# Optimization experiments

Measured on AMD Instinct MI355X. Metric: run time of the kernel, lower is better.

Reference implementation:

```python
import jax, jax.numpy as jnp
import numpy as np

K = 3                 # patch / kernel size (ksize)
SOFTMAX_SCALE = 10.0
RES_SCALE = 1.0
EPS = 1e-4            # escape_NaN


def prelu(x, a):
    # nn.PReLU() with a single learnable parameter a (shape [1])
    return jnp.where(x >= 0, x, a * x)


def conv1x1_prelu(x, w, b, a):
    # x: [N,C,H,W], w: [O,C], b: [O] -- 1x1 conv + PReLU (BasicBlock)
    y = jnp.einsum('nchw,oc->nohw', x, w) + b[None, :, None, None]
    return prelu(y, a)


def extract_patches(x):
    # SAME-padded 3x3 patch extraction, stride 1 (torch Unfold ordering: C,kh,kw)
    # x: [N,C,H,W] -> [N, H*W, C*9]
    N, C, H, W = x.shape
    xp = jnp.pad(x, ((0, 0), (0, 0), (1, 1), (1, 1)))
    p = jnp.stack([jnp.stack([xp[:, :, i:i + H, j:j + W] for j in range(K)], axis=2)
                   for i in range(K)], axis=2)          # [N,C,3,3,H,W] (i outer -> kh)
    return p.reshape(N, C * K * K, H * W).transpose(0, 2, 1)


def pyramid_attention(input_l, input_s, w_mlb, b_mlb, a_mlb, w_m, b_m, a_m, w_asm, b_asm, a_asm):
    N, _, H_l, W_l = input_l.shape
    _, _, H_s, W_s = input_s.shape
    L = H_s * W_s

    match_base = conv1x1_prelu(input_l, w_mlb, b_mlb, a_mlb)   # [N,32,H_l,W_l]
    base = conv1x1_prelu(input_s, w_asm, b_asm, a_asm)          # [N,64,H_s,W_s]
    ref = conv1x1_prelu(input_s, w_m, b_m, a_m)                 # [N,32,H_s,W_s]

    # key patches from ref, L2-normalized per patch (wi / (||wi|| + eps))
    w_patch = extract_patches(ref)                              # [N, L, 32*9]
    norm = jnp.sqrt(jnp.sum(w_patch * w_patch, axis=-1, keepdims=True)) + EPS
    w_normed = w_patch / norm

    # query patches from match_base (same padding), correlation == patch matmul
    x_patch = extract_patches(match_base)                       # [N, H_l*W_l, 32*9]
    scores = jnp.einsum('bpk,blk->bpl', x_patch, w_normed) * SOFTMAX_SCALE
    attn = jax.nn.softmax(scores, axis=-1)                      # softmax over L keys
    attn = attn.transpose(0, 2, 1).reshape(N, L, H_l, W_l)

    # value patches from base; conv_transpose2d(stride=1, padding=1) == conv with
    # spatially-flipped kernel and in/out channels swapped, SAME padding
    raw_w = extract_patches(base).reshape(N, L, 64, K, K)       # [N,L,64,3,3]
    w_ct = jnp.flip(raw_w, axis=(-2, -1)).transpose(0, 2, 1, 3, 4)  # [N,64,L,3,3]

    def per_sample(a, k):
        return jax.lax.conv_general_dilated(
            a[None], k, window_strides=(1, 1), padding=[(1, 1), (1, 1)],
            dimension_numbers=('NCHW', 'OIHW', 'NCHW'))[0]

    y = jax.vmap(per_sample)(attn, w_ct) / 4.0                  # [N,64,H_l,W_l]
    return y + input_l * RES_SCALE


def setup_inputs() -> dict:
    key = jax.random.key(0)
    ks = jax.random.split(key, 12)
    N, C, H_l, W_l, H_s, W_s = 4, 64, 96, 96, 48, 48
    Cr = C // 2  # reduction=2
    return {
        'input_l': jax.random.normal(ks[0], (N, C, H_l, W_l), jnp.float32),
        'input_s': jax.random.normal(ks[1], (N, C, H_s, W_s), jnp.float32),
        'w_mlb': jax.random.normal(ks[2], (Cr, C), jnp.float32) * 0.05,
        'b_mlb': jax.random.normal(ks[3], (Cr,), jnp.float32) * 0.01,
        'a_mlb': jnp.full((1,), 0.25, jnp.float32),
        'w_m': jax.random.normal(ks[4], (Cr, C), jnp.float32) * 0.05,
        'b_m': jax.random.normal(ks[5], (Cr,), jnp.float32) * 0.01,
        'a_m': jnp.full((1,), 0.25, jnp.float32),
        'w_asm': jax.random.normal(ks[6], (C, C), jnp.float32) * 0.05,
        'b_asm': jax.random.normal(ks[7], (C,), jnp.float32) * 0.01,
        'a_asm': jnp.full((1,), 0.25, jnp.float32),
    }


def reference(input_l, input_s, w_mlb, b_mlb, a_mlb, w_m, b_m, a_m, w_asm, b_asm, a_asm):
    return pyramid_attention(input_l, input_s, w_mlb, b_mlb, a_mlb,
                             w_m, b_m, a_m, w_asm, b_asm, a_asm)
```

## Files before the change

### kernel.cpp

```cpp
#include <hip/hip_runtime.h>
#include <hip/hip_bf16.h>
#include <cstdint>
#include <cstddef>

typedef __hip_bfloat16 bf16;
using short8 = __attribute__((ext_vector_type(8))) short;
using f32x4  = __attribute__((ext_vector_type(4))) float;
using float4v = __attribute__((ext_vector_type(4))) float;
using uint4v  = __attribute__((ext_vector_type(4))) unsigned int;

__device__ __forceinline__ float s2f(short s) {
  unsigned u = ((unsigned)(unsigned short)s) << 16;
  return __builtin_bit_cast(float, u);
}
__device__ __forceinline__ short f2s(float f) {
  unsigned u = __builtin_bit_cast(unsigned, f);
  u += 0x7fffu + ((u >> 16) & 1u);
  return (short)(u >> 16);
}
__device__ __forceinline__ float bclo(unsigned u) { return __builtin_bit_cast(float, u << 16); }
__device__ __forceinline__ float bchi(unsigned u) { return __builtin_bit_cast(float, u & 0xFFFF0000u); }

__global__ __launch_bounds__(256) void k_conv_all(
    const float* __restrict__ in_l, const float* __restrict__ in_s,
    const float* __restrict__ w_mlb, const float* __restrict__ b_mlb, const float* __restrict__ a_mlb,
    const float* __restrict__ w_m,   const float* __restrict__ b_m,   const float* __restrict__ a_m,
    const float* __restrict__ w_asm, const float* __restrict__ b_asm, const float* __restrict__ a_asm,
    float* __restrict__ MBpad, float* __restrict__ REFpad, float* __restrict__ BASEpad,
    int t1, int t2, int t3)
{
  int idx = blockIdx.x * 256 + threadIdx.x;
  const float *in, *w, *bi, *ap; float* o; int Cout, Hin, Win;
  if (idx < t1) { in = in_l; w = w_mlb; bi = b_mlb; ap = a_mlb; o = MBpad; Cout = 32; Hin = 96; Win = 96; }
  else if (idx < t1 + t2) { idx -= t1; in = in_s; w = w_m; bi = b_m; ap = a_m; o = REFpad; Cout = 32; Hin = 48; Win = 48; }
  else if (idx < t1 + t2 + t3) { idx -= t1 + t2; in = in_s; w = w_asm; bi = b_asm; ap = a_asm; o = BASEpad; Cout = 64; Hin = 48; Win = 48; }
  else return;
  int Wp = Win + 2, Hp = Hin + 2;
  int x = idx % Wp;
  int t = idx / Wp;
  int y = t % Hp; t /= Hp;
  int oc = t % Cout; int n = t / Cout;
  if (x == 0 || x == Wp - 1 || y == 0 || y == Hp - 1) { o[idx] = 0.0f; return; }
  int cs = Hin * Win;
  const float* ip = in + (size_t)n * 64 * cs + (size_t)(y - 1) * Win + (x - 1);
  const float* wp = w + oc * 64;
  float s = bi[oc];
#pragma unroll 16
  for (int ci = 0; ci < 64; ci++)
    s += wp[ci] * ip[(size_t)ci * cs];
  float a = ap[0];
  o[idx] = s >= 0.0f ? s : a * s;
}

__global__ __launch_bounds__(256) void k_gather_all(
    const float* __restrict__ mbpad, const float* __restrict__ refpad,
    const float* __restrict__ basepad,
    bf16* __restrict__ Kp, bf16* __restrict__ Xp, bf16* __restrict__ Bb)
{
  int b = blockIdx.x;
  int tid = threadIdx.x;
  if (b < 2304) {
    int wid = b * 4 + (tid >> 6);
    int lane = tid & 63;
    int n = wid / 2304, l = wid % 2304, lh = l / 48, lw = l % 48;
    float v[5]; float ss = 0.f;
#pragma unroll
    for (int i = 0; i < 5; i++) {
      int k = lane + 64 * i; v[i] = 0.f;
      if (k < 288) {
        int c = k / 9, rr = (k % 9) / 3, sc = k % 3;
        v[i] = refpad[((size_t)(n * 32 + c) * 50 + lh + rr) * 50 + lw + sc];
        ss += v[i] * v[i];
      }
    }
#pragma unroll
    for (int off = 32; off; off >>= 1) ss += __shfl_xor(ss, off);
    float inv = 10.f / (sqrtf(ss) + 1e-4f);
#pragma unroll
    for (int i = 0; i < 5; i++) {
      int k = lane + 64 * i;
      Kp[(size_t)wid * 320 + k] = __float2bfloat16(k < 288 ? v[i] * inv : 0.f);
    }
  } else if (b < 2304 + 46080) {
    int idx = (b - 2304) * 256 + tid;
    int k = idx % 320; int p = (idx / 320) % 9216; int n = idx / (320 * 9216);
    float val = 0.f;
    if (k < 288) {
      int c = k / 9, rr = (k % 9) / 3, sc = k % 3;
      int ph = p / 96, pw = p % 96;
      val = mbpad[((size_t)(n * 32 + c) * 98 + ph + rr) * 98 + pw + sc];
    }
    Xp[idx] = __float2bfloat16(val);
  } else {
    int idx = (b - 48384) * 256 + tid;
    int l = idx % 2304; int o = (idx / 2304) % 64; int n = idx / (2304 * 64);
    int lh = l / 48, lw = l % 48;
    Bb[idx] = __float2bfloat16(basepad[((size_t)(n * 64 + o) * 50 + lh + 1) * 50 + lw + 1]);
  }
}

__global__ __launch_bounds__(256, 3) void k_qk(
    const bf16* __restrict__ Xp, const bf16* __restrict__ Kp,
    bf16* __restrict__ attnT, float* __restrict__ statsM, float* __restrict__ statsZ,
    int nbase, int qlo)
{
  __shared__ __align__(16) short KsPs[256 * 72];
  __shared__ float Sm[2][2][32];
  __shared__ float Sz[2][2][32];
  int z = blockIdx.z;
  int n = nbase + z;
  attnT += (size_t)z * 9216 * 2304;
  statsM += (size_t)z * 9 * 9216;
  statsZ += (size_t)z * 9 * 9216;
  int tid = threadIdx.x, lane = tid & 63, wv = tid >> 6;
  int quad = lane >> 4, m16 = lane & 15;
  int wr = wv >> 1, wc = wv & 1;
  int q0 = qlo + blockIdx.x * 64;
  int l0 = blockIdx.y * 256;

  f32x4 acc[2][8];
#pragma unroll
  for (int mi = 0; mi < 2; mi++)
#pragma unroll
    for (int t = 0; t < 8; t++) acc[mi][t] = (f32x4){0.f, 0.f, 0.f, 0.f};

  const short* Xrow = (const short*)Xp + ((size_t)n * 9216 + q0 + wr * 32 + m16) * 320;
  const short* Ksrc = (const short*)Kp + ((size_t)n * 2304 + l0) * 320;
  int srow = tid >> 2;
  int scol = (tid & 3) * 16;

  short8 pf[8];
#pragma unroll
  for (int p = 0; p < 4; p++)
#pragma unroll
    for (int v = 0; v < 2; v++)
      pf[p * 2 + v] = *(const short8*)&Ksrc[(size_t)(srow + 64 * p) * 320 + scol + v * 8];

#pragma unroll
  for (int s = 0; s < 5; s++) {
    if (s) __syncthreads();
#pragma unroll
    for (int p = 0; p < 4; p++)
#pragma unroll
      for (int v = 0; v < 2; v++)
        *(short8*)&KsPs[(srow + 64 * p) * 72 + scol + v * 8] = pf[p * 2 + v];
    __syncthreads();
    short8 xa0 = *(const short8*)&Xrow[s * 64 + quad * 8];
    short8 xa1 = *(const short8*)&Xrow[16 * 320 + s * 64 + quad * 8];
    short8 xa2 = *(const short8*)&Xrow[s * 64 + 32 + quad * 8];
    short8 xa3 = *(const short8*)&Xrow[16 * 320 + s * 64 + 32 + quad * 8];
    if (s < 4) {
      int kn = (s + 1) * 64;
#pragma unroll
      for (int p = 0; p < 4; p++)
#pragma unroll
        for (int v = 0; v < 2; v++)
          pf[p * 2 + v] = *(const short8*)&Ksrc[(size_t)(srow + 64 * p) * 320 + kn + scol + v * 8];
    }
#pragma unroll
    for (int half = 0; half < 2; half++) {
      int kc = s * 64 + half * 32;
      if (kc >= 288) break;
      short8 a0 = half ? xa2 : xa0;
      short8 a1 = half ? xa3 : xa1;
#pragma unroll
      for (int t = 0; t < 8; t++) {
        short8 bfr = *(const short8*)&KsPs[(wc * 128 + t * 16 + m16) * 72 + half * 32 + quad * 8];
        acc[0][t] = __builtin_amdgcn_mfma_f32_16x16x32_bf16(a0, bfr, acc[0][t], 0, 0, 0);
        acc[1][t] = __builtin_amdgcn_mfma_f32_16x16x32_bf16(a1, bfr, acc[1][t], 0, 0, 0);
      }
    }
  }

  float mloc[2][4], zloc[2][4], scale[2][4];
#pragma unroll
  for (int mi = 0; mi < 2; mi++)
#pragma unroll
    for (int r = 0; r < 4; r++) mloc[mi][r] = -3.0e38f;
#pragma unroll
  for (int mi = 0; mi < 2; mi++)
#pragma unroll
    for (int t = 0; t < 8; t++)
#pragma unroll
      for (int r = 0; r < 4; r++) mloc[mi][r] = fmaxf(mloc[mi][r], acc[mi][t][r]);
#pragma unroll
  for (int off = 1; off < 16; off <<= 1)
#pragma unroll
    for (int mi = 0; mi < 2; mi++)
#pragma unroll
      for (int r = 0; r < 4; r++) mloc[mi][r] = fmaxf(mloc[mi][r], __shfl_xor(mloc[mi][r], off));
#pragma unroll
  for (int mi = 0; mi < 2; mi++)
#pragma unroll
    for (int r = 0; r < 4; r++) zloc[mi][r] = 0.f;
#pragma unroll
  for (int mi = 0; mi < 2; mi++)
#pragma unroll
    for (int t = 0; t < 8; t++)
#pragma unroll
      for (int r = 0; r < 4; r++) {
        float e = __expf(acc[mi][t][r] - mloc[mi][r]);
        acc[mi][t][r] = e;
        zloc[mi][r] += e;
      }
#pragma unroll
  for (int off = 1; off < 16; off <<= 1)
#pragma unroll
    for (int mi = 0; mi < 2; mi++)
#pragma unroll
      for (int r = 0; r < 4; r++) zloc[mi][r] += __shfl_xor(zloc[mi][r], off);
  if (m16 == 0) {
#pragma unroll
    for (int mi = 0; mi < 2; mi++)
#pragma unroll
      for (int r = 0; r < 4; r++) {
        int qi = mi * 16 + quad * 4 + r;
        Sm[wc][wr][qi] = mloc[mi][r];
        Sz[wc][wr][qi] = zloc[mi][r];
      }
  }
  __syncthreads();
#pragma unroll
  for (int mi = 0; mi < 2; mi++)
#pragma unroll
    for (int r = 0; r < 4; r++) {
      int qi = mi * 16 + quad * 4 + r;
      float mo = Sm[wc ^ 1][wr][qi];
      float zo = Sz[wc ^ 1][wr][qi];
      float mc = fmaxf(mloc[mi][r], mo);
      float sc = __expf(mloc[mi][r] - mc);
      scale[mi][r] = sc;
      if (m16 == 0 && wc == 0) {
        float zc = zloc[mi][r] * sc + zo * __expf(mo - mc);
        int qq = q0 + wr * 32 + qi;
        statsM[blockIdx.y * 9216 + qq] = mc;
        statsZ[blockIdx.y * 9216 + qq] = zc;
      }
    }
#pragma unroll
  for (int mi = 0; mi < 2; mi++)
#pragma unroll
    for (int t = 0; t < 8; t++)
#pragma unroll
      for (int r = 0; r < 4; r++)
        KsPs[(wr * 32 + mi * 16 + quad * 4 + r) * 264 + wc * 128 + t * 16 + m16] =
            f2s(acc[mi][t][r] * scale[mi][r]);
  __syncthreads();
  {
    int row = tid >> 2, part = tid & 3;
    short* dst = (short*)attnT + (size_t)(q0 - qlo + row) * 2304 + l0 + part * 64;
    const short* sp = &KsPs[row * 264 + part * 64];
#pragma unroll
    for (int v = 0; v < 8; v++)
      *(short8*)&dst[v * 8] = *(const short8*)&sp[v * 8];
  }
}

__global__ __launch_bounds__(256) void k_alpha(
    const float* __restrict__ statsM, const float* __restrict__ statsZ,
    float* __restrict__ alpha, int qlo, int qlen)
{
  int z = blockIdx.y;
  statsM += (size_t)z * 9 * 9216;
  statsZ += (size_t)z * 9 * 9216;
  alpha  += (size_t)z * 9 * 9216;
  int i = blockIdx.x * 256 + threadIdx.x;
  if (i >= qlen) return;
  int q = qlo + i;
  float M = -3.0e38f;
#pragma unroll
  for (int c = 0; c < 9; c++) M = fmaxf(M, statsM[c * 9216 + q]);
  float Z = 0.f;
#pragma unroll
  for (int c = 0; c < 9; c++) Z += statsZ[c * 9216 + q] * __expf(statsM[c * 9216 + q] - M);
  float invZ = 1.f / Z;
#pragma unroll
  for (int c = 0; c < 9; c++) alpha[c * 9216 + q] = __expf(statsM[c * 9216 + q] - M) * invZ;
}

__global__ __launch_bounds__(256) void k_a2(
    const bf16* __restrict__ attnT, const float* __restrict__ alpha,
    bf16* __restrict__ A2, int q0, int qlo)
{
  int z = blockIdx.z;
  attnT += (size_t)z * 9216 * 2304;
  alpha += (size_t)z * 9 * 9216;
  A2    += (size_t)z * 9216 * 2304;
  int bpx = gridDim.x >> 3;
  int nb = (blockIdx.x & 7) * bpx + (blockIdx.x >> 3);
  int g = nb * 256 + threadIdx.x;
  int qrel = g / 144;
  int j = g - qrel * 144;
  int l0 = j * 16;
  int q = q0 + qrel;
  int h = q / 96, w = q - h * 96;
  int lh = l0 / 48, lw0 = l0 - lh * 48;
  const short* att = (const short*)attnT;
  float acc[16];
#pragma unroll
  for (int k = 0; k < 16; k++) acc[k] = 0.f;
#pragma unroll
  for (int di = -1; di <= 1; di++) {
    int hh = h + di, lhh = lh + di;
    if (hh < 0 || hh >= 96 || lhh < 0 || lhh >= 48) continue;
    int lb = l0 + 48 * di;
    int qv = q + 96 * di;
    const short* r0 = att + (size_t)(qv - qlo) * 2304;
    int c0 = lb >> 8;
    const float* alc = alpha + c0 * 9216;
    {
      float a = alc[qv];
      uint4v Va = *(const uint4v*)(r0 + lb);
      uint4v Vb = *(const uint4v*)(r0 + lb + 8);
#pragma unroll
      for (int k = 0; k < 4; k++) {
        acc[2 * k]      += bclo(Va[k]) * a;  acc[2 * k + 1]  += bchi(Va[k]) * a;
        acc[8 + 2 * k]  += bclo(Vb[k]) * a;  acc[9 + 2 * k]  += bchi(Vb[k]) * a;
      }
    }
    if (w > 0) {
      const short* rm = r0 - 2304;
      int qp = qv - 1;
      float am = alc[qp];
      float a0 = ((lb & 255) == 0 && c0 > 0) ? alpha[(c0 - 1) * 9216 + qp] : am;
      uint4v Ma = *(const uint4v*)(rm + lb);
      uint4v Mb = *(const uint4v*)(rm + lb + 8);
      unsigned P = *(const unsigned*)(rm + lb - 2);
      unsigned D[8] = { Ma[0], Ma[1], Ma[2], Ma[3], Mb[0], Mb[1], Mb[2], Mb[3] };
      unsigned E0 = (P >> 16) | (D[0] << 16);
      if (lw0 == 0) E0 &= 0xFFFF0000u;
      acc[0] += bclo(E0) * a0;  acc[1] += bchi(E0) * am;
#pragma unroll
      for (int k = 1; k < 8; k++) {
        unsigned Ek = (D[k - 1] >> 16) | (D[k] << 16);
        acc[2 * k] += bclo(Ek) * am;  acc[2 * k + 1] += bchi(Ek) * am;
      }
    }
    if (w < 95) {
      const short* rp = r0 + 2304;
      int qp = qv + 1;
      float am = alc[qp];
      float a15 = ((lb & 255) == 240 && c0 < 8) ? alpha[(c0 + 1) * 9216 + qp] : am;
      uint4v Pa = *(const uint4v*)(rp + lb);
      uint4v Pb = *(const uint4v*)(rp + lb + 8);
      unsigned N = *(const unsigned*)(rp + lb + 16);
      unsigned D[9] = { Pa[0], Pa[1], Pa[2], Pa[3], Pb[0], Pb[1], Pb[2], Pb[3], N };
      unsigned F7 = (D[7] >> 16) | (D[8] << 16);
      if (lw0 == 32) F7 &= 0x0000FFFFu;
#pragma unroll
      for (int k = 0; k < 7; k++) {
        unsigned Fk = (D[k] >> 16) | (D[k + 1] << 16);
        acc[2 * k] += bclo(Fk) * am;  acc[2 * k + 1] += bchi(Fk) * am;
      }
      acc[14] += bclo(F7) * am;  acc[15] += bchi(F7) * a15;
    }
  }
  short8 o0, o1;
#pragma unroll
  for (int k = 0; k < 8; k++) { o0[k] = f2s(acc[k]); o1[k] = f2s(acc[8 + k]); }
  short* dst = (short*)A2 + (size_t)qrel * 2304 + l0;
  *(short8*)dst = o0;
  *(short8*)(dst + 8) = o1;
}

__global__ __launch_bounds__(256) void k_pv3(
    const bf16* __restrict__ A2, const bf16* __restrict__ Bb,
    const float* __restrict__ inl, float* __restrict__ out,
    int nbase, int q0base)
{
  __shared__ float Cred[4][16][67];
  int z = blockIdx.z;
  int n = nbase + z;
  A2 += (size_t)z * 9216 * 2304;
  int tid = threadIdx.x, lane = tid & 63, wv = tid >> 6;
  int quad = lane >> 4, m16 = lane & 15;
  int qb = blockIdx.x * 16;
  int kbase = wv * 576;
  f32x4 acc[4];
#pragma unroll
  for (int t = 0; t < 4; t++) acc[t] = (f32x4){0.f, 0.f, 0.f, 0.f};

  const short* Ap = (const short*)A2 + (size_t)qb * 2304 + kbase;
  const short* Bp = (const short*)Bb + (size_t)n * 64 * 2304 + kbase;

#pragma unroll
  for (int it = 0; it < 9; it++) {
    int kw = it * 64;
#pragma unroll
    for (int ks = 0; ks < 64; ks += 32) {
      short8 a = *(const short8*)&Ap[(size_t)m16 * 2304 + kw + ks + quad * 8];
#pragma unroll
      for (int ni = 0; ni < 4; ni++) {
        short8 b = *(const short8*)&Bp[(size_t)(ni * 16 + m16) * 2304 + kw + ks + quad * 8];
        acc[ni] = __builtin_amdgcn_mfma_f32_16x16x32_bf16(a, b, acc[ni], 0, 0, 0);
      }
    }
  }
#pragma unroll
  for (int ni = 0; ni < 4; ni++)
#pragma unroll
    for (int r = 0; r < 4; r++)
      Cred[wv][quad * 4 + r][ni * 16 + m16] = acc[ni][r];
  __syncthreads();
  {
    int o = tid >> 2;
    int qg = (tid & 3) * 4;
    float4v s;
#pragma unroll
    for (int j = 0; j < 4; j++)
      s[j] = Cred[0][qg + j][o] + Cred[1][qg + j][o] + Cred[2][qg + j][o] + Cred[3][qg + j][o];
    size_t oid = ((size_t)(n * 64 + o)) * 9216 + q0base + qb + qg;
    float4v r4 = *(const float4v*)&inl[oid];
    float4v y;
#pragma unroll
    for (int j = 0; j < 4; j++) y[j] = 0.25f * s[j] + r4[j];
    *(float4v*)&out[oid] = y;
  }
}

extern "C" void kernel_launch(void* const* d_in, const int* in_sizes, int n_in,
                              void* d_out, int out_size, void* d_ws, size_t ws_size,
                              hipStream_t stream)
{
  (void)in_sizes; (void)n_in; (void)out_size;
  const float* input_l = (const float*)d_in[0];
  const float* input_s = (const float*)d_in[1];
  const float* w_mlb = (const float*)d_in[2];
  const float* b_mlb = (const float*)d_in[3];
  const float* a_mlb = (const float*)d_in[4];
  const float* w_m   = (const float*)d_in[5];
  const float* b_m   = (const float*)d_in[6];
  const float* a_m   = (const float*)d_in[7];
  const float* w_asm = (const float*)d_in[8];
  const float* b_asm = (const float*)d_in[9];
  const float* a_asm = (const float*)d_in[10];
  float* out = (float*)d_out;

  char* base = (char*)d_ws;
  size_t off = 0;
  auto carve = [&](size_t bytes) -> char* {
    char* r = base + off;
    off += (bytes + 255) & ~(size_t)255;
    return r;
  };

  float* MBpad   = (float*)carve((size_t)4 * 32 * 98 * 98 * 4);
  float* REFpad  = (float*)carve((size_t)4 * 32 * 50 * 50 * 4);
  float* BASEpad = (float*)carve((size_t)4 * 64 * 50 * 50 * 4);
  bf16*  Kp      = (bf16*)carve((size_t)4 * 2304 * 320 * 2);
  bf16*  Xp      = (bf16*)carve((size_t)4 * 9216 * 320 * 2);
  bf16*  Bb      = (bf16*)carve((size_t)4 * 64 * 2304 * 2);
  float* statsM  = (float*)carve((size_t)2 * 9 * 9216 * 4);
  float* statsZ  = (float*)carve((size_t)2 * 9 * 9216 * 4);
  float* alpha   = (float*)carve((size_t)2 * 9 * 9216 * 4);
  size_t fixedOff = off;

  auto need = [&](int qmax, int psplit, int B) -> size_t {
    size_t a = (((size_t)qmax * 2304 * 2) * B + 255) & ~(size_t)255;
    size_t b2 = (((size_t)psplit * 2304 * 2) * B + 255) & ~(size_t)255;
    return fixedOff + a + b2;
  };
  int nsplit, qmax, psplit, batchB;
  if (need(9216, 9216, 2) <= ws_size)      { batchB = 2; nsplit = 1; qmax = 9216; psplit = 9216; }
  else if (need(9216, 9216, 1) <= ws_size) { batchB = 1; nsplit = 1; qmax = 9216; psplit = 9216; }
  else if (need(5120, 4608, 1) <= ws_size) { batchB = 1; nsplit = 2; qmax = 5120; psplit = 4608; }
  else                                     { batchB = 1; nsplit = 4; qmax = 2816; psplit = 2304; }

  bf16* attnT = (bf16*)carve((size_t)qmax * 2304 * 2 * batchB);
  bf16* A2    = (bf16*)carve((size_t)psplit * 2304 * 2 * batchB);

  {
    int t1 = 4 * 32 * 98 * 98;
    int t2 = 4 * 32 * 50 * 50;
    int t3 = 4 * 64 * 50 * 50;
    int tt = t1 + t2 + t3;
    k_conv_all<<<dim3((tt + 255) / 256), dim3(256), 0, stream>>>(
        input_l, input_s, w_mlb, b_mlb, a_mlb, w_m, b_m, a_m, w_asm, b_asm, a_asm,
        MBpad, REFpad, BASEpad, t1, t2, t3);
    k_gather_all<<<dim3(2304 + 46080 + 2304), dim3(256), 0, stream>>>(
        MBpad, REFpad, BASEpad, Kp, Xp, Bb);
  }

  if (batchB == 2) {
    for (int p = 0; p < 2; p++) {
      int nb = p * 2;
      k_qk<<<dim3(144, 9, 2), dim3(256), 0, stream>>>(Xp, Kp, attnT, statsM, statsZ, nb, 0);
      k_alpha<<<dim3(36, 2), dim3(256), 0, stream>>>(statsM, statsZ, alpha, 0, 9216);
      k_a2<<<dim3(5184, 1, 2), dim3(256), 0, stream>>>(attnT, alpha, A2, 0, 0);
      k_pv3<<<dim3(576, 1, 2), dim3(256), 0, stream>>>(A2, Bb, input_l, out, nb, 0);
    }
  } else {
    for (int n = 0; n < 4; n++) {
      for (int s = 0; s < nsplit; s++) {
        int q0 = s * psplit;
        int qlo = q0 - 256; if (qlo < 0) qlo = 0;
        int qhi = q0 + psplit + 256; if (qhi > 9216) qhi = 9216;
        int qlen = qhi - qlo;
        k_qk<<<dim3(qlen / 64, 9, 1), dim3(256), 0, stream>>>(Xp, Kp, attnT, statsM, statsZ, n, qlo);
        k_alpha<<<dim3(qlen / 256, 1), dim3(256), 0, stream>>>(statsM, statsZ, alpha, qlo, qlen);
        k_a2<<<dim3(psplit * 144 / 256, 1, 1), dim3(256), 0, stream>>>(attnT, alpha, A2, q0, qlo);
        k_pv3<<<dim3(psplit / 16, 1, 1), dim3(256), 0, stream>>>(A2, Bb, input_l, out, n, q0);
      }
    }
  }
}
```

Measured before the change: 526.5 us.

## Split PV reduction across blocks with atomics, vectorize gathers, prefetch Q fragments

The PV kernel's K reduction is split over two blocks along grid.y, and each block now atomically adds its scaled partial into an output that a new residual-copy kernel pre-initializes with input_l. The X and B gather paths each write eight bf16 values per thread as a vector store instead of one scalar each. The QK kernel loads the next stage's X fragments after the MFMA loop so the global load latency overlaps compute. Together these aim to raise PV occupancy and cut gather store traffic, at the cost of atomic contention, an extra output pass, and nondeterministic summation order.

New measurement: 526.4 us. Within noise of the previous version (-0.0%).

```diff
diff --git a/kernel.cpp b/kernel.cpp
--- a/kernel.cpp
+++ b/kernel.cpp
@@ -20,6 +20,9 @@
 }
 __device__ __forceinline__ float bclo(unsigned u) { return __builtin_bit_cast(float, u << 16); }
 __device__ __forceinline__ float bchi(unsigned u) { return __builtin_bit_cast(float, u & 0xFFFF0000u); }
+__device__ __forceinline__ short bfbits(float f) {
+  return __builtin_bit_cast(short, __float2bfloat16(f));
+}
 
 __global__ __launch_bounds__(256) void k_conv_all(
     const float* __restrict__ in_l, const float* __restrict__ in_s,
@@ -52,6 +55,14 @@
   o[idx] = s >= 0.0f ? s : a * s;
 }
 
+__global__ __launch_bounds__(256) void k_resid(
+    const float* __restrict__ inl, float* __restrict__ out, int total4)
+{
+  int i = blockIdx.x * 256 + threadIdx.x;
+  if (i < total4)
+    ((float4v*)out)[i] = ((const float4v*)inl)[i];
+}
+
 __global__ __launch_bounds__(256) void k_gather_all(
     const float* __restrict__ mbpad, const float* __restrict__ refpad,
     const float* __restrict__ basepad,
@@ -81,21 +92,34 @@
       int k = lane + 64 * i;
       Kp[(size_t)wid * 320 + k] = __float2bfloat16(k < 288 ? v[i] * inv : 0.f);
     }
-  } else if (b < 2304 + 46080) {
+  } else if (b < 2304 + 5760) {
     int idx = (b - 2304) * 256 + tid;
-    int k = idx % 320; int p = (idx / 320) % 9216; int n = idx / (320 * 9216);
-    float val = 0.f;
-    if (k < 288) {
-      int c = k / 9, rr = (k % 9) / 3, sc = k % 3;
+    int g = idx % 40;
+    int p = (idx / 40) % 9216;
+    int n = idx / (40 * 9216);
+    short8 v8 = (short8){0, 0, 0, 0, 0, 0, 0, 0};
+    if (g < 36) {
       int ph = p / 96, pw = p % 96;
-      val = mbpad[((size_t)(n * 32 + c) * 98 + ph + rr) * 98 + pw + sc];
-    }
-    Xp[idx] = __float2bfloat16(val);
+#pragma unroll
+      for (int j = 0; j < 8; j++) {
+        int k = g * 8 + j;
+        int c = k / 9, rr = (k % 9) / 3, sc = k % 3;
+        v8[j] = bfbits(mbpad[((size_t)(n * 32 + c) * 98 + ph + rr) * 98 + pw + sc]);
+      }
+    }
+    *(short8*)((short*)Xp + (size_t)idx * 8) = v8;
   } else {
-    int idx = (b - 48384) * 256 + tid;
-    int l = idx % 2304; int o = (idx / 2304) % 64; int n = idx / (2304 * 64);
-    int lh = l / 48, lw = l % 48;
-    Bb[idx] = __float2bfloat16(basepad[((size_t)(n * 64 + o) * 50 + lh + 1) * 50 + lw + 1]);
+    int idx = (b - 2304 - 5760) * 256 + tid;
+    int l8 = idx % 288;
+    int o = (idx / 288) % 64;
+    int n = idx / (288 * 64);
+    int l0 = l8 * 8;
+    int lh = l0 / 48, lw = l0 % 48;
+    const float* src = &basepad[((size_t)(n * 64 + o) * 50 + lh + 1) * 50 + lw + 1];
+    short8 v8;
+#pragma unroll
+    for (int j = 0; j < 8; j++) v8[j] = bfbits(src[j]);
+    *(short8*)((short*)Bb + (size_t)idx * 8) = v8;
   }
 }
 
@@ -135,6 +159,10 @@
 #pragma unroll
     for (int v = 0; v < 2; v++)
       pf[p * 2 + v] = *(const short8*)&Ksrc[(size_t)(srow + 64 * p) * 320 + scol + v * 8];
+  short8 xa0 = *(const short8*)&Xrow[quad * 8];
+  short8 xa1 = *(const short8*)&Xrow[16 * 320 + quad * 8];
+  short8 xa2 = *(const short8*)&Xrow[32 + quad * 8];
+  short8 xa3 = *(const short8*)&Xrow[16 * 320 + 32 + quad * 8];
 
 #pragma unroll
   for (int s = 0; s < 5; s++) {
@@ -145,10 +173,6 @@
       for (int v = 0; v < 2; v++)
         *(short8*)&KsPs[(srow + 64 * p) * 72 + scol + v * 8] = pf[p * 2 + v];
     __syncthreads();
-    short8 xa0 = *(const short8*)&Xrow[s * 64 + quad * 8];
-    short8 xa1 = *(const short8*)&Xrow[16 * 320 + s * 64 + quad * 8];
-    short8 xa2 = *(const short8*)&Xrow[s * 64 + 32 + quad * 8];
-    short8 xa3 = *(const short8*)&Xrow[16 * 320 + s * 64 + 32 + quad * 8];
     if (s < 4) {
       int kn = (s + 1) * 64;
 #pragma unroll
@@ -169,6 +193,13 @@
         acc[0][t] = __builtin_amdgcn_mfma_f32_16x16x32_bf16(a0, bfr, acc[0][t], 0, 0, 0);
         acc[1][t] = __builtin_amdgcn_mfma_f32_16x16x32_bf16(a1, bfr, acc[1][t], 0, 0, 0);
       }
+    }
+    if (s < 4) {
+      int kn = (s + 1) * 64;
+      xa0 = *(const short8*)&Xrow[kn + quad * 8];
+      xa1 = *(const short8*)&Xrow[16 * 320 + kn + quad * 8];
+      xa2 = *(const short8*)&Xrow[kn + 32 + quad * 8];
+      xa3 = *(const short8*)&Xrow[16 * 320 + kn + 32 + quad * 8];
     }
   }
 
@@ -365,8 +396,7 @@
 
 __global__ __launch_bounds__(256) void k_pv3(
     const bf16* __restrict__ A2, const bf16* __restrict__ Bb,
-    const float* __restrict__ inl, float* __restrict__ out,
-    int nbase, int q0base)
+    float* __restrict__ out, int nbase, int q0base)
 {
   __shared__ float Cred[4][16][67];
   int z = blockIdx.z;
@@ -375,7 +405,7 @@
   int tid = threadIdx.x, lane = tid & 63, wv = tid >> 6;
   int quad = lane >> 4, m16 = lane & 15;
   int qb = blockIdx.x * 16;
-  int kbase = wv * 576;
+  int kbase = blockIdx.y * 1152 + wv * 288;
   f32x4 acc[4];
 #pragma unroll
   for (int t = 0; t < 4; t++) acc[t] = (f32x4){0.f, 0.f, 0.f, 0.f};
@@ -385,15 +415,12 @@
 
 #pragma unroll
   for (int it = 0; it < 9; it++) {
-    int kw = it * 64;
-#pragma unroll
-    for (int ks = 0; ks < 64; ks += 32) {
-      short8 a = *(const short8*)&Ap[(size_t)m16 * 2304 + kw + ks + quad * 8];
-#pragma unroll
-      for (int ni = 0; ni < 4; ni++) {
-        short8 b = *(const short8*)&Bp[(size_t)(ni * 16 + m16) * 2304 + kw + ks + quad * 8];
-        acc[ni] = __builtin_amdgcn_mfma_f32_16x16x32_bf16(a, b, acc[ni], 0, 0, 0);
-      }
+    int kw = it * 32;
+    short8 a = *(const short8*)&Ap[(size_t)m16 * 2304 + kw + quad * 8];
+#pragma unroll
+    for (int ni = 0; ni < 4; ni++) {
+      short8 b = *(const short8*)&Bp[(size_t)(ni * 16 + m16) * 2304 + kw + quad * 8];
+      acc[ni] = __builtin_amdgcn_mfma_f32_16x16x32_bf16(a, b, acc[ni], 0, 0, 0);
     }
   }
 #pragma unroll
@@ -405,16 +432,12 @@
   {
     int o = tid >> 2;
     int qg = (tid & 3) * 4;
-    float4v s;
-#pragma unroll
-    for (int j = 0; j < 4; j++)
-      s[j] = Cred[0][qg + j][o] + Cred[1][qg + j][o] + Cred[2][qg + j][o] + Cred[3][qg + j][o];
     size_t oid = ((size_t)(n * 64 + o)) * 9216 + q0base + qb + qg;
-    float4v r4 = *(const float4v*)&inl[oid];
-    float4v y;
-#pragma unroll
-    for (int j = 0; j < 4; j++) y[j] = 0.25f * s[j] + r4[j];
-    *(float4v*)&out[oid] = y;
+#pragma unroll
+    for (int j = 0; j < 4; j++) {
+      float s = Cred[0][qg + j][o] + Cred[1][qg + j][o] + Cred[2][qg + j][o] + Cred[3][qg + j][o];
+      atomicAdd(&out[oid + j], 0.25f * s);
+    }
   }
 }
 
@@ -477,7 +500,8 @@
     k_conv_all<<<dim3((tt + 255) / 256), dim3(256), 0, stream>>>(
         input_l, input_s, w_mlb, b_mlb, a_mlb, w_m, b_m, a_m, w_asm, b_asm, a_asm,
         MBpad, REFpad, BASEpad, t1, t2, t3);
-    k_gather_all<<<dim3(2304 + 46080 + 2304), dim3(256), 0, stream>>>(
+    k_resid<<<dim3(2304), dim3(256), 0, stream>>>(input_l, out, 4 * 64 * 9216 / 4);
+    k_gather_all<<<dim3(2304 + 5760 + 288), dim3(256), 0, stream>>>(
         MBpad, REFpad, BASEpad, Kp, Xp, Bb);
   }
 
@@ -487,7 +511,7 @@
       k_qk<<<dim3(144, 9, 2), dim3(256), 0, stream>>>(Xp, Kp, attnT, statsM, statsZ, nb, 0);
       k_alpha<<<dim3(36, 2), dim3(256), 0, stream>>>(statsM, statsZ, alpha, 0, 9216);
       k_a2<<<dim3(5184, 1, 2), dim3(256), 0, stream>>>(attnT, alpha, A2, 0, 0);
-      k_pv3<<<dim3(576, 1, 2), dim3(256), 0, stream>>>(A2, Bb, input_l, out, nb, 0);
+      k_pv3<<<dim3(576, 2, 2), dim3(256), 0, stream>>>(A2, Bb, out, nb, 0);
     }
   } else {
     for (int n = 0; n < 4; n++) {
@@ -499,8 +523,8 @@
         k_qk<<<dim3(qlen / 64, 9, 1), dim3(256), 0, stream>>>(Xp, Kp, attnT, statsM, statsZ, n, qlo);
         k_alpha<<<dim3(qlen / 256, 1), dim3(256), 0, stream>>>(statsM, statsZ, alpha, qlo, qlen);
         k_a2<<<dim3(psplit * 144 / 256, 1, 1), dim3(256), 0, stream>>>(attnT, alpha, A2, q0, qlo);
-        k_pv3<<<dim3(psplit / 16, 1, 1), dim3(256), 0, stream>>>(A2, Bb, input_l, out, n, q0);
-      }
-    }
-  }
-}
+        k_pv3<<<dim3(psplit / 16, 2, 1), dim3(256), 0, stream>>>(A2, Bb, out, n, q0);
+      }
+    }
+  }
+}
```
